# Performance work log

Hardware: AMD Instinct MI355X
Metric: run time of the kernel (lower is better)

## Reference

```python
import jax, jax.numpy as jnp
import numpy as np


def _lstm(x, Wih, Whh, b):
    # x: [B, T, D]; torch gate order (i, f, g, o); returns final (h, c)
    B = x.shape[0]
    H = Whh.shape[0]
    def step(carry, xt):
        h, c = carry
        gates = xt @ Wih + h @ Whh + b
        i, f, g, o = jnp.split(gates, 4, axis=-1)
        c = jax.nn.sigmoid(f) * c + jax.nn.sigmoid(i) * jnp.tanh(g)
        h = jax.nn.sigmoid(o) * jnp.tanh(c)
        return (h, c), None
    h0 = jnp.zeros((B, H), x.dtype)
    (h, c), _ = jax.lax.scan(step, (h0, h0), jnp.swapaxes(x, 0, 1))
    return h, c


def _bn(x, g, b, eps=1e-5):
    # BatchNorm1d training-mode math (biased variance over batch dim)
    m = x.mean(0)
    v = x.var(0)
    return (x - m) * jax.lax.rsqrt(v + eps) * g + b


def setup_inputs():
    L, N, C, D, H, HID = 16, 128, 10, 13, 128, 64
    F = 15 + 7 + 2 + HID  # 88, lstm2/composer input width
    key = jax.random.key(0)
    ks = jax.random.split(key, 20)
    def rn(i, shape, s=0.08):
        return jax.random.normal(ks[i], shape, jnp.float32) * s
    return {
        "operators": rn(0, (L, N, 15), 1.0),
        "extra_infos": rn(1, (L, N, 7), 1.0),
        "cardinalities": rn(2, (L, N, 2), 1.0),
        "condition1s": rn(3, (L, N, C, D), 1.0),
        "condition2s": rn(4, (L, N, C, D), 1.0),
        "mapping": jax.random.randint(ks[5], (L - 1, N, 2), 0, N + 1, jnp.int32),
        # lstm1
        "Wih1": rn(6, (D, 4 * H)), "Whh1": rn(7, (H, 4 * H)), "b1": jnp.zeros((4 * H,), jnp.float32),
        # condition_mlp + batch_norm1
        "Wc": rn(8, (H, HID)), "bc": jnp.zeros((HID,), jnp.float32),
        "g1": jnp.ones((HID,), jnp.float32), "be1": jnp.zeros((HID,), jnp.float32),
        # lstm2
        "Wih2": rn(9, (F, 4 * H)), "Whh2": rn(10, (H, 4 * H)), "b2": jnp.zeros((4 * H,), jnp.float32),
        # composer: input proj + 5 stacked (lh, rh) gate Linears, order [i, lf, rf, u, o]
        "Win": rn(11, (F, H)), "bin_": jnp.zeros((H,), jnp.float32),
        "Wlh": rn(12, (5, H, H)), "blh": jnp.zeros((5, H), jnp.float32),
        "Wrh": rn(13, (5, H, H)), "brh": jnp.zeros((5, H), jnp.float32),
        # head (task1 only; task2 branch is dead code in forward)
        "g2": jnp.ones((H,), jnp.float32), "be2": jnp.zeros((H,), jnp.float32),
        "Wt1": rn(14, (H, HID)), "bt1": jnp.zeros((HID,), jnp.float32),
        "g3": jnp.ones((HID,), jnp.float32), "be3": jnp.zeros((HID,), jnp.float32),
        "Wt2": rn(15, (HID, HID)), "bt2": jnp.zeros((HID,), jnp.float32),
        "Wo": rn(16, (HID, 1)), "bo": jnp.zeros((1,), jnp.float32),
    }


def _forward(operators, extra_infos, cardinalities, condition1s, condition2s, mapping,
             Wih1, Whh1, b1, Wc, bc, g1, be1, Wih2, Whh2, b2,
             Win, bin_, Wlh, blh, Wrh, brh,
             g2, be2, Wt1, bt1, g3, be3, Wt2, bt2, Wo, bo):
    L, N = operators.shape[0], operators.shape[1]
    H = Whh1.shape[0]
    # condition encoder: both condition tensors share lstm1 -> run batched together
    C, D = condition1s.shape[2], condition1s.shape[3]
    c_all = jnp.concatenate([condition1s, condition2s], 0).reshape(2 * L * N, C, D)
    h_all, _ = _lstm(c_all, Wih1, Whh1, b1)
    h1, h2 = jnp.split(h_all, 2, 0)
    lo = (jax.nn.relu(h1 @ Wc + bc) + jax.nn.relu(h2 @ Wc + bc)) * 0.5
    lo = _bn(lo, g1, be1).reshape(L, N, -1)
    out = jnp.concatenate([operators, extra_infos, cardinalities, lo], 2)  # [L, N, F]

    # leaf level through lstm2 (seq len 1, zero init)
    h0, c0 = _lstm(out[L - 1][:, None, :], Wih2, Whh2, b2)  # [N, H]
    # torch code broadcasts [N,1,H] input against [*,N,H] hidden -> state is [N,N,H];
    # pre-broadcasting the initial [1,N,H] state to [N,N,H] is value-identical and lets us scan.
    hid = jnp.broadcast_to(h0[None], (N, N, H))
    cid = jnp.broadcast_to(c0[None], (N, N, H))

    def step(carry, x):
        hid, cid = carry
        lvl, mp = x  # lvl: [N, F], mp: [N, 2] with values in [0, N] (0 = zero pad)
        pad = jnp.zeros((N, 1, H), hid.dtype)
        nh = jnp.concatenate([pad, hid], 1)  # [N, N+1, H]
        nc = jnp.concatenate([pad, cid], 1)
        lh, lc = nh[:, mp[:, 0]], nc[:, mp[:, 0]]  # [N, N, H]
        rh, rc = nh[:, mp[:, 1]], nc[:, mp[:, 1]]
        base = (lvl @ Win + bin_)[:, None, :]  # [N, 1, H] (computed once, reused for all 5 gates)
        pre = (base[None]
               + jnp.einsum('anh,ghk->gank', lh, Wlh) + blh[:, None, None, :]
               + jnp.einsum('anh,ghk->gank', rh, Wrh) + brh[:, None, None, :])  # [5, N, N, H]
        i = jax.nn.sigmoid(pre[0])
        lf = jax.nn.sigmoid(pre[1])
        rf = jax.nn.sigmoid(pre[2])
        u = jnp.tanh(pre[3])
        o = jax.nn.sigmoid(pre[4])
        c = i * u + lf * lc + rf * rc
        h = o * jnp.tanh(c)
        return (h, c), None

    (hid, cid), _ = jax.lax.scan(step, (hid, cid), (out[:L - 1][::-1], mapping[::-1]))
    output = hid[0]  # [N, H]; original slices [0:batch_size]=N here (randn operators are nonzero)
    t = _bn(output, g2, be2)
    t = jax.nn.relu(t @ Wt1 + bt1)
    t = _bn(t, g3, be3)
    t = jax.nn.relu(t @ Wt2 + bt2)
    return jax.nn.sigmoid(t @ Wo + bo)  # [N, 1]


def reference(operators, extra_infos, cardinalities, condition1s, condition2s, mapping,
              Wih1, Whh1, b1, Wc, bc, g1, be1, Wih2, Whh2, b2,
              Win, bin_, Wlh, blh, Wrh, brh,
              g2, be2, Wt1, bt1, g3, be3, Wt2, bt2, Wo, bo):
    return _forward(operators, extra_infos, cardinalities, condition1s, condition2s, mapping,
                    Wih1, Whh1, b1, Wc, bc, g1, be1, Wih2, Whh2, b2,
                    Win, bin_, Wlh, blh, Wrh, brh,
                    g2, be2, Wt1, bt1, g3, be3, Wt2, bt2, Wo, bo)
```

## Files before the change

kernel.cpp:

```cpp
#include <hip/hip_runtime.h>
#include <hip/hip_bf16.h>

__device__ __forceinline__ float sigf(float x) {
  return __fdividef(1.0f, 1.0f + __expf(-x));
}
__device__ __forceinline__ float tanhfast(float x) {
  float e = __expf(2.0f * x);
  return 1.0f - __fdividef(2.0f, e + 1.0f);
}

__global__ __launch_bounds__(256) void k_pre(
    const float* __restrict__ Whh1, const float* __restrict__ Wih1,
    const float* __restrict__ b1, const float* __restrict__ Wlh,
    const float* __restrict__ Wrh,
    float* __restrict__ WhhP, float* __restrict__ WihP,
    float* __restrict__ b1P, float* __restrict__ WT)
{
  const int bx = blockIdx.x, tid = threadIdx.x;
  if (bx < 32) {
    for (int i = 0; i < 8; ++i) {
      int dst = bx * 2048 + i * 256 + tid;
      int g = dst & 3, u = (dst >> 2) & 127, k = dst >> 9;
      WhhP[dst] = Whh1[k * 512 + g * 128 + u];
    }
  } else if (bx == 32) {
    for (int idx = tid; idx < 13 * 512; idx += 256) {
      int g = idx & 3, u = (idx >> 2) & 127, d = idx >> 9;
      WihP[idx] = Wih1[d * 512 + g * 128 + u];
    }
    for (int idx = tid; idx < 512; idx += 256)
      b1P[idx] = b1[(idx & 3) * 128 + (idx >> 2)];
  } else {
    __shared__ float tile[32][33];
    const int m = bx - 33;
    const int side = m / 5, g = m - side * 5;
    const float* src = (side ? Wrh : Wlh) + g * 16384;
    float* dst = WT + m * 16384;
    const int i = tid >> 5, jj = tid & 31;
    for (int tt = 0; tt < 16; ++tt) {
      const int ti = tt >> 2, tj = tt & 3;
#pragma unroll
      for (int q = 0; q < 4; ++q)
        tile[i + q * 8][jj] = src[(ti * 32 + i + q * 8) * 128 + tj * 32 + jj];
      __syncthreads();
#pragma unroll
      for (int q = 0; q < 4; ++q)
        dst[(tj * 32 + i + q * 8) * 128 + ti * 32 + jj] = tile[jj][i + q * 8];
      __syncthreads();
    }
  }
}

__global__ __launch_bounds__(512, 1) void k_lstm1(
    const float* __restrict__ cond1, const float* __restrict__ cond2,
    const float* __restrict__ WihP, const float* __restrict__ WhhP,
    const float* __restrict__ b1P, const float* __restrict__ Wc,
    const float* __restrict__ bc,
    float* __restrict__ lo_raw, float* __restrict__ gpartial)
{
  __shared__ float4 pS[4][8][128];
  __shared__ float4 hs4[16][32];
  __shared__ float  xs[16][132];
  __shared__ float4 WihS[13][128];
  __shared__ float  rr[16][64];
  __shared__ float  sloc[128];

  const int tid = threadIdx.x, b = blockIdx.x;
  const int u = tid & 127, rg = tid >> 7;

  for (int idx = tid; idx < 16 * 130; idx += 512) {
    int r = idx / 130, d = idx - r * 130;
    xs[r][d] = (r < 8) ? cond1[(8 * b + r) * 130 + d]
                       : cond2[(8 * b + (r - 8)) * 130 + d];
  }
  for (int idx = tid; idx < 13 * 128; idx += 512)
    WihS[idx >> 7][idx & 127] =
        *(const float4*)&WihP[(idx >> 7) * 512 + 4 * (idx & 127)];
  ((float4*)hs4)[tid] = make_float4(0.f, 0.f, 0.f, 0.f);
  if (tid < 128) sloc[tid] = 0.f;

  float4 w[32];
#pragma unroll
  for (int kk = 0; kk < 32; ++kk)
    w[kk] = *(const float4*)&WhhP[(32 * rg + kk) * 512 + 4 * u];
  const float4 b1v = *(const float4*)&b1P[4 * u];
  float creg[4] = {0.f, 0.f, 0.f, 0.f};
  __syncthreads();

  for (int t = 0; t < 10; ++t) {
#pragma unroll
    for (int hf = 0; hf < 2; ++hf) {
      const int base = 8 * hf;
#pragma unroll
      for (int row = 0; row < 8; ++row) {
        float4 a = make_float4(0.f, 0.f, 0.f, 0.f);
#pragma unroll
        for (int q = 0; q < 8; ++q) {
          const float4 hv = hs4[base + row][8 * rg + q];
          const float4 w0 = w[4 * q + 0], w1 = w[4 * q + 1];
          const float4 w2 = w[4 * q + 2], w3 = w[4 * q + 3];
          a.x = fmaf(hv.x, w0.x, a.x); a.y = fmaf(hv.x, w0.y, a.y);
          a.z = fmaf(hv.x, w0.z, a.z); a.w = fmaf(hv.x, w0.w, a.w);
          a.x = fmaf(hv.y, w1.x, a.x); a.y = fmaf(hv.y, w1.y, a.y);
          a.z = fmaf(hv.y, w1.z, a.z); a.w = fmaf(hv.y, w1.w, a.w);
          a.x = fmaf(hv.z, w2.x, a.x); a.y = fmaf(hv.z, w2.y, a.y);
          a.z = fmaf(hv.z, w2.z, a.z); a.w = fmaf(hv.z, w2.w, a.w);
          a.x = fmaf(hv.w, w3.x, a.x); a.y = fmaf(hv.w, w3.y, a.y);
          a.z = fmaf(hv.w, w3.z, a.z); a.w = fmaf(hv.w, w3.w, a.w);
        }
        pS[rg][row][u] = a;
      }
      __syncthreads();
      {
        float4 gs[2];
#pragma unroll
        for (int i = 0; i < 2; ++i) {
          const int rh = 2 * rg + i;
          float4 s0 = pS[0][rh][u], s1 = pS[1][rh][u];
          float4 s2 = pS[2][rh][u], s3 = pS[3][rh][u];
          gs[i].x = ((s0.x + s1.x) + (s2.x + s3.x)) + b1v.x;
          gs[i].y = ((s0.y + s1.y) + (s2.y + s3.y)) + b1v.y;
          gs[i].z = ((s0.z + s1.z) + (s2.z + s3.z)) + b1v.z;
          gs[i].w = ((s0.w + s1.w) + (s2.w + s3.w)) + b1v.w;
        }
#pragma unroll
        for (int d = 0; d < 13; ++d) {
          const float4 wv = WihS[d][u];
#pragma unroll
          for (int i = 0; i < 2; ++i) {
            const float xv = xs[base + 2 * rg + i][t * 13 + d];
            gs[i].x = fmaf(xv, wv.x, gs[i].x);
            gs[i].y = fmaf(xv, wv.y, gs[i].y);
            gs[i].z = fmaf(xv, wv.z, gs[i].z);
            gs[i].w = fmaf(xv, wv.w, gs[i].w);
          }
        }
#pragma unroll
        for (int i = 0; i < 2; ++i) {
          const int row = base + 2 * rg + i;
          const int ci = 2 * hf + i;
          float ig = sigf(gs[i].x);
          float fg = sigf(gs[i].y);
          float gg = tanhfast(gs[i].z);
          float og = sigf(gs[i].w);
          float c = fmaf(fg, creg[ci], ig * gg);
          creg[ci] = c;
          ((float*)&hs4[row][0])[u] = og * tanhfast(c);
        }
      }
      __syncthreads();
    }
  }

  {
    const int oc = tid & 63, r8 = tid >> 6;
    const float* h0 = (const float*)&hs4[2 * r8][0];
    const float* h1 = (const float*)&hs4[2 * r8 + 1][0];
    float a0 = bc[oc], a1 = a0;
    for (int k = 0; k < 128; ++k) {
      float wcv = Wc[k * 64 + oc];
      a0 = fmaf(h0[k], wcv, a0);
      a1 = fmaf(h1[k], wcv, a1);
    }
    rr[2 * r8][oc] = fmaxf(a0, 0.f);
    rr[2 * r8 + 1][oc] = fmaxf(a1, 0.f);
  }
  __syncthreads();
  {
    const int j = tid >> 6, oc = tid & 63;
    float lo = 0.5f * (rr[j][oc] + rr[j + 8][oc]);
    lo_raw[(8 * b + j) * 64 + oc] = lo;
    atomicAdd(&sloc[oc], lo);
    atomicAdd(&sloc[64 + oc], lo * lo);
  }
  __syncthreads();
  if (tid < 128) gpartial[tid * 256 + b] = sloc[tid];
}

__device__ __forceinline__ void bn1_scales(
    const float* __restrict__ gpartial, const float* __restrict__ g1,
    const float* __restrict__ be1, float* sS, float* av, float* bv)
{
  const int tid = threadIdx.x;
  if (tid < 128) {
    const float4* gp = (const float4*)(gpartial + tid * 256);
    float s = 0.f;
    for (int i = 0; i < 64; ++i) {
      float4 v = gp[i];
      s += (v.x + v.y) + (v.z + v.w);
    }
    sS[tid] = s;
  }
  __syncthreads();
  if (tid < 64) {
    float m = sS[tid] * (1.0f / 2048.0f);
    float var = sS[64 + tid] * (1.0f / 2048.0f) - m * m;
    float rstd = rsqrtf(var + 1e-5f);
    float gg = g1[tid];
    av[tid] = rstd * gg;
    bv[tid] = be1[tid] - m * rstd * gg;
  }
  __syncthreads();
}

__device__ __forceinline__ float feat(
    int l, int n, int f, const float* __restrict__ ops,
    const float* __restrict__ extra, const float* __restrict__ card,
    const float* __restrict__ lo_raw, const float* av, const float* bv)
{
  int g = l * 128 + n;
  if (f < 15) return ops[g * 15 + f];
  if (f < 22) return extra[g * 7 + (f - 15)];
  if (f < 24) return card[g * 2 + (f - 22)];
  int j = f - 24;
  return lo_raw[g * 64 + j] * av[j] + bv[j];
}

__global__ __launch_bounds__(256) void k_mid(
    const float* __restrict__ ops, const float* __restrict__ extra,
    const float* __restrict__ card, const float* __restrict__ lo_raw,
    const float* __restrict__ gpartial, const float* __restrict__ g1,
    const float* __restrict__ be1, const float* __restrict__ Wih2,
    const float* __restrict__ b2, const float* __restrict__ Win,
    const float* __restrict__ binb, float* __restrict__ hidA,
    float* __restrict__ cidA, float* __restrict__ base_all)
{
  __shared__ float sS[128], av[64], bv[64];
  __shared__ float X[2][88];
  const int tid = threadIdx.x, bx = blockIdx.x;
  bn1_scales(gpartial, g1, be1, sS, av, bv);

  if (bx < 64) {
    if (tid < 176) {
      int r = tid / 88, f = tid - r * 88;
      X[r][f] = feat(15, 2 * bx + r, f, ops, extra, card, lo_raw, av, bv);
    }
    __syncthreads();
    const int nl = tid >> 7, k = tid & 127;
    const float* Xr = X[nl];
    float ai = b2[k];
    float ag = b2[256 + k];
    float ao = b2[384 + k];
#pragma unroll 8
    for (int f = 0; f < 88; ++f) {
      float xv = Xr[f];
      ai = fmaf(xv, Wih2[f * 512 + k], ai);
      ag = fmaf(xv, Wih2[f * 512 + 256 + k], ag);
      ao = fmaf(xv, Wih2[f * 512 + 384 + k], ao);
    }
    float c0 = sigf(ai) * tanhfast(ag);
    float h0 = sigf(ao) * tanhfast(c0);
    const int idx = (2 * bx + nl) * 128 + k;
    hidA[idx] = h0;
    cidA[idx] = c0;
  } else {
    const int t = bx - 64;
    if (tid < 88)
      X[0][tid] = feat(t, 0, tid, ops, extra, card, lo_raw, av, bv);
    __syncthreads();
    if (tid < 128) {
      float a = binb[tid];
#pragma unroll 8
      for (int f = 0; f < 88; ++f)
        a = fmaf(X[0][f], Win[f * 128 + tid], a);
      base_all[t * 128 + tid] = a;
    }
  }
}

__global__ __launch_bounds__(512, 1) void k_tree(
    const int* __restrict__ mapping, const float* __restrict__ WT,
    const float* __restrict__ base_all, const float* __restrict__ blh,
    const float* __restrict__ brh, const float* __restrict__ hid_c,
    const float* __restrict__ cid_c, float* __restrict__ hid_n,
    float* __restrict__ cid_n, int t)
{
  __shared__ float wS[10][8][132];
  __shared__ float rowS[64][132];
  __shared__ float pS[10][264];
  const int tid = threadIdx.x, bx = blockIdx.x;
  const int k0 = (bx & 15) * 8, n0 = (bx >> 4) * 32;

  for (int idx = tid; idx < 10 * 8 * 128; idx += 512) {
    int h = idx & 127, kp = (idx >> 7) & 7, sg = idx >> 10;
    wS[sg][kp][h] = WT[sg * 16384 + (k0 + kp) * 128 + h];
  }
  for (int idx = tid; idx < 64 * 128; idx += 512) {
    int row = idx >> 7, h = idx & 127;
    int np_ = row >> 1, side = row & 1;
    int j = mapping[(t * 128 + n0 + np_) * 2 + side];
    rowS[row][h] = (j > 0) ? hid_c[(j - 1) * 128 + h] : 0.0f;
  }
  __syncthreads();

  {
    const int pr = tid >> 1, side = tid & 1;
    const int np_ = pr >> 3, kp = pr & 7;
    const int rrow = np_ * 2 + side;
    float acc[5] = {0.f, 0.f, 0.f, 0.f, 0.f};
    for (int h = 0; h < 128; h += 8) {
      float4 r0 = *(const float4*)&rowS[rrow][h];
      float4 r1 = *(const float4*)&rowS[rrow][h + 4];
#pragma unroll
      for (int g = 0; g < 5; ++g) {
        float4 w0 = *(const float4*)&wS[side * 5 + g][kp][h];
        float4 w1 = *(const float4*)&wS[side * 5 + g][kp][h + 4];
        acc[g] = fmaf(r0.x, w0.x, acc[g]);
        acc[g] = fmaf(r0.y, w0.y, acc[g]);
        acc[g] = fmaf(r0.z, w0.z, acc[g]);
        acc[g] = fmaf(r0.w, w0.w, acc[g]);
        acc[g] = fmaf(r1.x, w1.x, acc[g]);
        acc[g] = fmaf(r1.y, w1.y, acc[g]);
        acc[g] = fmaf(r1.z, w1.z, acc[g]);
        acc[g] = fmaf(r1.w, w1.w, acc[g]);
      }
    }
#pragma unroll
    for (int g = 0; g < 5; ++g) pS[side * 5 + g][pr] = acc[g];
  }
  __syncthreads();
  if (tid < 256) {
    const int np_ = tid >> 3, kp = tid & 7;
    const int n = n0 + np_, k = k0 + kp;
    const float base = base_all[t * 128 + k];
    float pre[5];
#pragma unroll
    for (int g = 0; g < 5; ++g)
      pre[g] = pS[g][tid] + pS[5 + g][tid] + base +
               blh[g * 128 + k] + brh[g * 128 + k];
    int jl = mapping[(t * 128 + n) * 2 + 0];
    int jr = mapping[(t * 128 + n) * 2 + 1];
    float lc = (jl > 0) ? cid_c[(jl - 1) * 128 + k] : 0.0f;
    float rc = (jr > 0) ? cid_c[(jr - 1) * 128 + k] : 0.0f;
    float i_ = sigf(pre[0]);
    float lf = sigf(pre[1]);
    float rf = sigf(pre[2]);
    float u_ = tanhfast(pre[3]);
    float o_ = sigf(pre[4]);
    float c = i_ * u_ + lf * lc + rf * rc;
    hid_n[n * 128 + k] = o_ * tanhfast(c);
    cid_n[n * 128 + k] = c;
  }
}

__global__ __launch_bounds__(512) void k_head(
    const float* __restrict__ hid, const float* __restrict__ g2,
    const float* __restrict__ be2, const float* __restrict__ Wt1,
    const float* __restrict__ bt1, const float* __restrict__ g3,
    const float* __restrict__ be3, const float* __restrict__ Wt2,
    const float* __restrict__ bt2, const float* __restrict__ Wo,
    const float* __restrict__ bo, float* __restrict__ dout)
{
  __shared__ __align__(16) unsigned char pool[32768 + 16384];
  __hip_bfloat16 (*t1s)[128] = (__hip_bfloat16(*)[128])pool;
  __hip_bfloat16 (*t2s)[64]  = (__hip_bfloat16(*)[64])(pool + 32768);
  float (*t4s)[64] = (float(*)[64])pool;
  __shared__ float red[8][128];
  __shared__ float av[128], bv[128];
  const int tid = threadIdx.x;

  {
    int k = tid & 127, q = tid >> 7;
    float s = 0.f, s2 = 0.f;
    for (int r = q * 32; r < q * 32 + 32; ++r) {
      float v = hid[r * 128 + k];
      s += v; s2 += v * v;
    }
    red[q][k] = s;
    red[4 + q][k] = s2;
  }
  __syncthreads();
  if (tid < 128) {
    float s = red[0][tid] + red[1][tid] + red[2][tid] + red[3][tid];
    float s2 = red[4][tid] + red[5][tid] + red[6][tid] + red[7][tid];
    float m = s * (1.0f / 128.0f);
    float var = s2 * (1.0f / 128.0f) - m * m;
    float rstd = rsqrtf(var + 1e-5f);
    float gg = g2[tid];
    av[tid] = rstd * gg;
    bv[tid] = be2[tid] - m * rstd * gg;
  }
  __syncthreads();
  for (int idx = tid; idx < 16384; idx += 512) {
    int n = idx >> 7, k = idx & 127;
    t1s[n][k] = __float2bfloat16(hid[idx] * av[k] + bv[k]);
  }
  __syncthreads();
  {
    const int j = tid & 63, ng = tid >> 6;
    float a[16];
#pragma unroll
    for (int r = 0; r < 16; ++r) a[r] = bt1[j];
    for (int k8 = 0; k8 < 128; k8 += 8) {
      float wv[8];
#pragma unroll
      for (int q = 0; q < 8; ++q) wv[q] = Wt1[(k8 + q) * 64 + j];
#pragma unroll
      for (int r = 0; r < 16; ++r) {
        const __hip_bfloat16* row = &t1s[ng * 16 + r][k8];
#pragma unroll
        for (int q = 0; q < 8; ++q)
          a[r] = fmaf(__bfloat162float(row[q]), wv[q], a[r]);
      }
    }
#pragma unroll
    for (int r = 0; r < 16; ++r)
      t2s[ng * 16 + r][j] = __float2bfloat16(fmaxf(a[r], 0.0f));
  }
  __syncthreads();
  {
    int j = tid & 63, q = tid >> 6;
    float s = 0.f, s2 = 0.f;
    for (int r = q * 16; r < q * 16 + 16; ++r) {
      float v = __bfloat162float(t2s[r][j]);
      s += v; s2 += v * v;
    }
    red[q][j] = s;
    red[q][64 + j] = s2;
  }
  __syncthreads();
  if (tid < 64) {
    float s = 0.f, s2 = 0.f;
#pragma unroll
    for (int q = 0; q < 8; ++q) { s += red[q][tid]; s2 += red[q][64 + tid]; }
    float m = s * (1.0f / 128.0f);
    float var = s2 * (1.0f / 128.0f) - m * m;
    float rstd = rsqrtf(var + 1e-5f);
    float gg = g3[tid];
    av[tid] = rstd * gg;
    bv[tid] = be3[tid] - m * rstd * gg;
  }
  __syncthreads();
  {
    const int j2 = tid & 63, ng = tid >> 6;
    float a[16];
#pragma unroll
    for (int r = 0; r < 16; ++r) a[r] = bt2[j2];
    for (int jj = 0; jj < 64; ++jj) {
      float w = Wt2[jj * 64 + j2];
      float aj = av[jj], bj = bv[jj];
#pragma unroll
      for (int r = 0; r < 16; ++r) {
        float x = __bfloat162float(t2s[ng * 16 + r][jj]) * aj + bj;
        a[r] = fmaf(x, w, a[r]);
      }
    }
    __syncthreads();
#pragma unroll
    for (int r = 0; r < 16; ++r) t4s[ng * 16 + r][j2] = fmaxf(a[r], 0.0f);
  }
  __syncthreads();
  if (tid < 128) {
    float a = bo[0];
    for (int j = 0; j < 64; ++j) a = fmaf(t4s[tid][j], Wo[j], a);
    dout[tid] = sigf(a);
  }
}

extern "C" void kernel_launch(void* const* d_in, const int* in_sizes, int n_in,
                              void* d_out, int out_size, void* d_ws,
                              size_t ws_size, hipStream_t stream)
{
  (void)in_sizes; (void)n_in; (void)out_size; (void)ws_size;
  const float* ops   = (const float*)d_in[0];
  const float* extra = (const float*)d_in[1];
  const float* card  = (const float*)d_in[2];
  const float* cond1 = (const float*)d_in[3];
  const float* cond2 = (const float*)d_in[4];
  const int* mapping = (const int*)d_in[5];
  const float* Wih1 = (const float*)d_in[6];
  const float* Whh1 = (const float*)d_in[7];
  const float* b1   = (const float*)d_in[8];
  const float* Wc   = (const float*)d_in[9];
  const float* bc   = (const float*)d_in[10];
  const float* g1   = (const float*)d_in[11];
  const float* be1  = (const float*)d_in[12];
  const float* Wih2 = (const float*)d_in[13];
  const float* b2   = (const float*)d_in[15];
  const float* Win  = (const float*)d_in[16];
  const float* binb = (const float*)d_in[17];
  const float* Wlh  = (const float*)d_in[18];
  const float* blh  = (const float*)d_in[19];
  const float* Wrh  = (const float*)d_in[20];
  const float* brh  = (const float*)d_in[21];
  const float* g2   = (const float*)d_in[22];
  const float* be2  = (const float*)d_in[23];
  const float* Wt1  = (const float*)d_in[24];
  const float* bt1  = (const float*)d_in[25];
  const float* g3   = (const float*)d_in[26];
  const float* be3  = (const float*)d_in[27];
  const float* Wt2  = (const float*)d_in[28];
  const float* bt2  = (const float*)d_in[29];
  const float* Wo   = (const float*)d_in[30];
  const float* bo   = (const float*)d_in[31];

  char* ws = (char*)d_ws;
  float* WhhP     = (float*)(ws + 0);
  float* WihP     = (float*)(ws + 262144);
  float* b1P      = (float*)(ws + 288768);
  float* gpartial = (float*)(ws + 290816);
  float* lo_raw   = (float*)(ws + 421888);
  float* base_all = (float*)(ws + 946176);
  float* WT       = (float*)(ws + 953856);
  float* hidA     = (float*)(ws + 1609216);
  float* hidB     = hidA + 16384;
  float* cidA     = hidB + 16384;
  float* cidB     = cidA + 16384;

  k_pre<<<dim3(43), dim3(256), 0, stream>>>(
      Whh1, Wih1, b1, Wlh, Wrh, WhhP, WihP, b1P, WT);
  k_lstm1<<<dim3(256), dim3(512), 0, stream>>>(
      cond1, cond2, WihP, WhhP, b1P, Wc, bc, lo_raw, gpartial);
  k_mid<<<dim3(79), dim3(256), 0, stream>>>(
      ops, extra, card, lo_raw, gpartial, g1, be1, Wih2, b2, Win, binb,
      hidA, cidA, base_all);

  float* hc[2] = {hidA, hidB};
  float* cc[2] = {cidA, cidB};
  for (int s = 0; s < 15; ++s) {
    int t = 14 - s;
    int cur = s & 1, nxt = cur ^ 1;
    k_tree<<<dim3(64), dim3(512), 0, stream>>>(
        mapping, WT, base_all, blh, brh,
        hc[cur], cc[cur], hc[nxt], cc[nxt], t);
  }
  k_head<<<dim3(1), dim3(512), 0, stream>>>(
      hc[1], g2, be2, Wt1, bt1, g3, be3, Wt2, bt2, Wo, bo,
      (float*)d_out);
}
```

Before: 445.3 us.

## Move LSTM1 recurrence onto bf16 split-precision MFMA and simplify tree kernel reduction

```diff
diff --git a/kernel.cpp b/kernel.cpp
--- a/kernel.cpp
+++ b/kernel.cpp
@@ -1,5 +1,9 @@
 #include <hip/hip_runtime.h>
 #include <hip/hip_bf16.h>
+
+typedef __attribute__((ext_vector_type(8))) short short8v;
+typedef __attribute__((ext_vector_type(4))) short short4v;
+typedef __attribute__((ext_vector_type(4))) float f32x4;
 
 __device__ __forceinline__ float sigf(float x) {
   return __fdividef(1.0f, 1.0f + __expf(-x));
@@ -8,31 +12,39 @@
   float e = __expf(2.0f * x);
   return 1.0f - __fdividef(2.0f, e + 1.0f);
 }
+__device__ __forceinline__ unsigned short rne_bf16(float x) {
+  unsigned u = __float_as_uint(x);
+  return (unsigned short)((u + 0x7fffu + ((u >> 16) & 1u)) >> 16);
+}
+__device__ __forceinline__ float bf2f(unsigned short s) {
+  return __uint_as_float(((unsigned)s) << 16);
+}
 
 __global__ __launch_bounds__(256) void k_pre(
     const float* __restrict__ Whh1, const float* __restrict__ Wih1,
-    const float* __restrict__ b1, const float* __restrict__ Wlh,
-    const float* __restrict__ Wrh,
-    float* __restrict__ WhhP, float* __restrict__ WihP,
-    float* __restrict__ b1P, float* __restrict__ WT)
+    const float* __restrict__ Wlh, const float* __restrict__ Wrh,
+    unsigned short* __restrict__ Bft, float* __restrict__ WT)
 {
   const int bx = blockIdx.x, tid = threadIdx.x;
-  if (bx < 32) {
-    for (int i = 0; i < 8; ++i) {
-      int dst = bx * 2048 + i * 256 + tid;
-      int g = dst & 3, u = (dst >> 2) & 127, k = dst >> 9;
-      WhhP[dst] = Whh1[k * 512 + g * 128 + u];
-    }
-  } else if (bx == 32) {
-    for (int idx = tid; idx < 13 * 512; idx += 256) {
-      int g = idx & 3, u = (idx >> 2) & 127, d = idx >> 9;
-      WihP[idx] = Wih1[d * 512 + g * 128 + u];
-    }
-    for (int idx = tid; idx < 512; idx += 256)
-      b1P[idx] = b1[(idx & 3) * 128 + (idx >> 2)];
+  if (bx < 40) {
+    for (int i = 0; i < 16; ++i) {
+      int idx = (bx * 256 + tid) * 16 + i;
+      int p = (idx >= 81920) ? 1 : 0;
+      int r = idx - p * 81920;
+      int q = r >> 14;
+      int rem = r & 16383;
+      int ct = rem >> 9, l = (rem >> 3) & 63, e = rem & 7;
+      int kk = 32 * q + ((l >> 4) << 3) + e;
+      int col = (ct << 4) + (l & 15);
+      float x = 0.f;
+      if (kk < 128) x = Whh1[kk * 512 + col];
+      else if (kk < 141) x = Wih1[(kk - 128) * 512 + col];
+      unsigned short hi = rne_bf16(x);
+      Bft[idx] = p ? rne_bf16(x - bf2f(hi)) : hi;
+    }
   } else {
     __shared__ float tile[32][33];
-    const int m = bx - 33;
+    const int m = bx - 40;
     const int side = m / 5, g = m - side * 5;
     const float* src = (side ? Wrh : Wlh) + g * 16384;
     float* dst = WT + m * 16384;
@@ -53,114 +65,146 @@
 
 __global__ __launch_bounds__(512, 1) void k_lstm1(
     const float* __restrict__ cond1, const float* __restrict__ cond2,
-    const float* __restrict__ WihP, const float* __restrict__ WhhP,
-    const float* __restrict__ b1P, const float* __restrict__ Wc,
-    const float* __restrict__ bc,
+    const unsigned short* __restrict__ Bft, const float* __restrict__ b1,
+    const float* __restrict__ Wc, const float* __restrict__ bc,
     float* __restrict__ lo_raw, float* __restrict__ gpartial)
 {
-  __shared__ float4 pS[4][8][128];
-  __shared__ float4 hs4[16][32];
-  __shared__ float  xs[16][132];
-  __shared__ float4 WihS[13][128];
-  __shared__ float  rr[16][64];
-  __shared__ float  sloc[128];
+  __shared__ __align__(16) unsigned short AftS[2][5][64][8];
+  __shared__ float preS[16][516];
+  __shared__ float xs[16][132];
+  __shared__ float hsF[16][132];
+  __shared__ float rr[16][64];
+  __shared__ float sloc[128];
 
   const int tid = threadIdx.x, b = blockIdx.x;
-  const int u = tid & 127, rg = tid >> 7;
+  const int wid = tid >> 6, lane = tid & 63;
 
   for (int idx = tid; idx < 16 * 130; idx += 512) {
     int r = idx / 130, d = idx - r * 130;
     xs[r][d] = (r < 8) ? cond1[(8 * b + r) * 130 + d]
                        : cond2[(8 * b + (r - 8)) * 130 + d];
   }
-  for (int idx = tid; idx < 13 * 128; idx += 512)
-    WihS[idx >> 7][idx & 127] =
-        *(const float4*)&WihP[(idx >> 7) * 512 + 4 * (idx & 127)];
-  ((float4*)hs4)[tid] = make_float4(0.f, 0.f, 0.f, 0.f);
+  for (int idx = tid; idx < 2560; idx += 512) ((unsigned*)AftS)[idx] = 0u;
   if (tid < 128) sloc[tid] = 0.f;
 
-  float4 w[32];
-#pragma unroll
-  for (int kk = 0; kk < 32; ++kk)
-    w[kk] = *(const float4*)&WhhP[(32 * rg + kk) * 512 + 4 * u];
-  const float4 b1v = *(const float4*)&b1P[4 * u];
+  short8v Bh[5][4], Bl[5][4];
+  {
+    const short8v* gB = (const short8v*)Bft;
+#pragma unroll
+    for (int q = 0; q < 5; ++q)
+#pragma unroll
+      for (int j = 0; j < 4; ++j) {
+        int ct = 4 * wid + j;
+        Bh[q][j] = gB[(q * 32 + ct) * 64 + lane];
+        Bl[q][j] = gB[((5 + q) * 32 + ct) * 64 + lane];
+      }
+  }
+  float biasv[4];
+#pragma unroll
+  for (int j = 0; j < 4; ++j) biasv[j] = b1[(4 * wid + j) * 16 + (lane & 15)];
+
+  const int grow = tid >> 5;
+  const int guu = (tid & 31) * 4;
   float creg[4] = {0.f, 0.f, 0.f, 0.f};
+
+  __syncthreads();
+  if (tid < 256) {
+    int p = tid >> 7, s = tid & 127, row = s & 15, grp = s >> 4;
+    {
+      float v = xs[row][grp];
+      unsigned short hi = rne_bf16(v);
+      AftS[p][4][row][grp] = p ? rne_bf16(v - bf2f(hi)) : hi;
+    }
+    if (grp < 5) {
+      float v = xs[row][8 + grp];
+      unsigned short hi = rne_bf16(v);
+      AftS[p][4][16 + row][grp] = p ? rne_bf16(v - bf2f(hi)) : hi;
+    }
+  }
   __syncthreads();
 
   for (int t = 0; t < 10; ++t) {
-#pragma unroll
-    for (int hf = 0; hf < 2; ++hf) {
-      const int base = 8 * hf;
-#pragma unroll
-      for (int row = 0; row < 8; ++row) {
-        float4 a = make_float4(0.f, 0.f, 0.f, 0.f);
-#pragma unroll
-        for (int q = 0; q < 8; ++q) {
-          const float4 hv = hs4[base + row][8 * rg + q];
-          const float4 w0 = w[4 * q + 0], w1 = w[4 * q + 1];
-          const float4 w2 = w[4 * q + 2], w3 = w[4 * q + 3];
-          a.x = fmaf(hv.x, w0.x, a.x); a.y = fmaf(hv.x, w0.y, a.y);
-          a.z = fmaf(hv.x, w0.z, a.z); a.w = fmaf(hv.x, w0.w, a.w);
-          a.x = fmaf(hv.y, w1.x, a.x); a.y = fmaf(hv.y, w1.y, a.y);
-          a.z = fmaf(hv.y, w1.z, a.z); a.w = fmaf(hv.y, w1.w, a.w);
-          a.x = fmaf(hv.z, w2.x, a.x); a.y = fmaf(hv.z, w2.y, a.y);
-          a.z = fmaf(hv.z, w2.z, a.z); a.w = fmaf(hv.z, w2.w, a.w);
-          a.x = fmaf(hv.w, w3.x, a.x); a.y = fmaf(hv.w, w3.y, a.y);
-          a.z = fmaf(hv.w, w3.z, a.z); a.w = fmaf(hv.w, w3.w, a.w);
-        }
-        pS[rg][row][u] = a;
-      }
-      __syncthreads();
+    f32x4 acc[4];
+#pragma unroll
+    for (int j = 0; j < 4; ++j)
+      acc[j] = (f32x4){biasv[j], biasv[j], biasv[j], biasv[j]};
+#pragma unroll
+    for (int q = 0; q < 5; ++q) {
+      short8v ah = *(const short8v*)&AftS[0][q][lane][0];
+      short8v al = *(const short8v*)&AftS[1][q][lane][0];
+#pragma unroll
+      for (int j = 0; j < 4; ++j) {
+        acc[j] = __builtin_amdgcn_mfma_f32_16x16x32_bf16(al, Bh[q][j],
+                                                         acc[j], 0, 0, 0);
+        acc[j] = __builtin_amdgcn_mfma_f32_16x16x32_bf16(ah, Bl[q][j],
+                                                         acc[j], 0, 0, 0);
+        acc[j] = __builtin_amdgcn_mfma_f32_16x16x32_bf16(ah, Bh[q][j],
+                                                         acc[j], 0, 0, 0);
+      }
+    }
+#pragma unroll
+    for (int j = 0; j < 4; ++j) {
+      int c = (4 * wid + j) * 16 + (lane & 15);
+      int r0 = (lane >> 4) * 4;
+#pragma unroll
+      for (int r = 0; r < 4; ++r) preS[r0 + r][c] = acc[j][r];
+    }
+    __syncthreads();
+    {
+      float4 pi = *(const float4*)&preS[grow][0 * 128 + guu];
+      float4 pf = *(const float4*)&preS[grow][1 * 128 + guu];
+      float4 pg = *(const float4*)&preS[grow][2 * 128 + guu];
+      float4 po = *(const float4*)&preS[grow][3 * 128 + guu];
+      float hv[4];
+#pragma unroll
+      for (int i2 = 0; i2 < 4; ++i2) {
+        float ig = sigf(((const float*)&pi)[i2]);
+        float fg = sigf(((const float*)&pf)[i2]);
+        float gg = tanhfast(((const float*)&pg)[i2]);
+        float og = sigf(((const float*)&po)[i2]);
+        float c = fmaf(fg, creg[i2], ig * gg);
+        creg[i2] = c;
+        hv[i2] = og * tanhfast(c);
+      }
+      *(float4*)&hsF[grow][guu] = make_float4(hv[0], hv[1], hv[2], hv[3]);
+      unsigned short h0 = rne_bf16(hv[0]), h1 = rne_bf16(hv[1]);
+      unsigned short h2 = rne_bf16(hv[2]), h3 = rne_bf16(hv[3]);
+      short4v hiv = (short4v){(short)h0, (short)h1, (short)h2, (short)h3};
+      short4v lov = (short4v){(short)rne_bf16(hv[0] - bf2f(h0)),
+                              (short)rne_bf16(hv[1] - bf2f(h1)),
+                              (short)rne_bf16(hv[2] - bf2f(h2)),
+                              (short)rne_bf16(hv[3] - bf2f(h3))};
+      int chunk = guu >> 5;
+      int lA = grow + 16 * ((guu >> 3) & 3);
+      int e0 = guu & 7;
+      *(short4v*)&AftS[0][chunk][lA][e0] = hiv;
+      *(short4v*)&AftS[1][chunk][lA][e0] = lov;
+    }
+    if (t < 9 && tid < 256) {
+      int p = tid >> 7, s = tid & 127, row = s & 15, grp = s >> 4;
       {
-        float4 gs[2];
-#pragma unroll
-        for (int i = 0; i < 2; ++i) {
-          const int rh = 2 * rg + i;
-          float4 s0 = pS[0][rh][u], s1 = pS[1][rh][u];
-          float4 s2 = pS[2][rh][u], s3 = pS[3][rh][u];
-          gs[i].x = ((s0.x + s1.x) + (s2.x + s3.x)) + b1v.x;
-          gs[i].y = ((s0.y + s1.y) + (s2.y + s3.y)) + b1v.y;
-          gs[i].z = ((s0.z + s1.z) + (s2.z + s3.z)) + b1v.z;
-          gs[i].w = ((s0.w + s1.w) + (s2.w + s3.w)) + b1v.w;
-        }
-#pragma unroll
-        for (int d = 0; d < 13; ++d) {
-          const float4 wv = WihS[d][u];
-#pragma unroll
-          for (int i = 0; i < 2; ++i) {
-            const float xv = xs[base + 2 * rg + i][t * 13 + d];
-            gs[i].x = fmaf(xv, wv.x, gs[i].x);
-            gs[i].y = fmaf(xv, wv.y, gs[i].y);
-            gs[i].z = fmaf(xv, wv.z, gs[i].z);
-            gs[i].w = fmaf(xv, wv.w, gs[i].w);
-          }
-        }
-#pragma unroll
-        for (int i = 0; i < 2; ++i) {
-          const int row = base + 2 * rg + i;
-          const int ci = 2 * hf + i;
-          float ig = sigf(gs[i].x);
-          float fg = sigf(gs[i].y);
-          float gg = tanhfast(gs[i].z);
-          float og = sigf(gs[i].w);
-          float c = fmaf(fg, creg[ci], ig * gg);
-          creg[ci] = c;
-          ((float*)&hs4[row][0])[u] = og * tanhfast(c);
-        }
-      }
-      __syncthreads();
-    }
+        float v = xs[row][(t + 1) * 13 + grp];
+        unsigned short hi = rne_bf16(v);
+        AftS[p][4][row][grp] = p ? rne_bf16(v - bf2f(hi)) : hi;
+      }
+      if (grp < 5) {
+        float v = xs[row][(t + 1) * 13 + 8 + grp];
+        unsigned short hi = rne_bf16(v);
+        AftS[p][4][16 + row][grp] = p ? rne_bf16(v - bf2f(hi)) : hi;
+      }
+    }
+    __syncthreads();
   }
 
   {
     const int oc = tid & 63, r8 = tid >> 6;
-    const float* h0 = (const float*)&hs4[2 * r8][0];
-    const float* h1 = (const float*)&hs4[2 * r8 + 1][0];
+    const float* h0p = &hsF[2 * r8][0];
+    const float* h1p = &hsF[2 * r8 + 1][0];
     float a0 = bc[oc], a1 = a0;
     for (int k = 0; k < 128; ++k) {
       float wcv = Wc[k * 64 + oc];
-      a0 = fmaf(h0[k], wcv, a0);
-      a1 = fmaf(h1[k], wcv, a1);
+      a0 = fmaf(h0p[k], wcv, a0);
+      a1 = fmaf(h1p[k], wcv, a1);
     }
     rr[2 * r8][oc] = fmaxf(a0, 0.f);
     rr[2 * r8 + 1][oc] = fmaxf(a1, 0.f);
@@ -277,15 +321,14 @@
 {
   __shared__ float wS[10][8][132];
   __shared__ float rowS[64][132];
-  __shared__ float pS[10][264];
   const int tid = threadIdx.x, bx = blockIdx.x;
   const int k0 = (bx & 15) * 8, n0 = (bx >> 4) * 32;
 
-  for (int idx = tid; idx < 10 * 8 * 128; idx += 512) {
+  for (int idx = tid; idx < 10240; idx += 512) {
     int h = idx & 127, kp = (idx >> 7) & 7, sg = idx >> 10;
     wS[sg][kp][h] = WT[sg * 16384 + (k0 + kp) * 128 + h];
   }
-  for (int idx = tid; idx < 64 * 128; idx += 512) {
+  for (int idx = tid; idx < 8192; idx += 512) {
     int row = idx >> 7, h = idx & 127;
     int np_ = row >> 1, side = row & 1;
     int j = mapping[(t * 128 + n0 + np_) * 2 + side];
@@ -293,51 +336,48 @@
   }
   __syncthreads();
 
-  {
-    const int pr = tid >> 1, side = tid & 1;
-    const int np_ = pr >> 3, kp = pr & 7;
-    const int rrow = np_ * 2 + side;
-    float acc[5] = {0.f, 0.f, 0.f, 0.f, 0.f};
-    for (int h = 0; h < 128; h += 8) {
-      float4 r0 = *(const float4*)&rowS[rrow][h];
-      float4 r1 = *(const float4*)&rowS[rrow][h + 4];
-#pragma unroll
-      for (int g = 0; g < 5; ++g) {
-        float4 w0 = *(const float4*)&wS[side * 5 + g][kp][h];
-        float4 w1 = *(const float4*)&wS[side * 5 + g][kp][h + 4];
-        acc[g] = fmaf(r0.x, w0.x, acc[g]);
-        acc[g] = fmaf(r0.y, w0.y, acc[g]);
-        acc[g] = fmaf(r0.z, w0.z, acc[g]);
-        acc[g] = fmaf(r0.w, w0.w, acc[g]);
-        acc[g] = fmaf(r1.x, w1.x, acc[g]);
-        acc[g] = fmaf(r1.y, w1.y, acc[g]);
-        acc[g] = fmaf(r1.z, w1.z, acc[g]);
-        acc[g] = fmaf(r1.w, w1.w, acc[g]);
-      }
-    }
-#pragma unroll
-    for (int g = 0; g < 5; ++g) pS[side * 5 + g][pr] = acc[g];
-  }
-  __syncthreads();
-  if (tid < 256) {
-    const int np_ = tid >> 3, kp = tid & 7;
-    const int n = n0 + np_, k = k0 + kp;
-    const float base = base_all[t * 128 + k];
-    float pre[5];
-#pragma unroll
-    for (int g = 0; g < 5; ++g)
-      pre[g] = pS[g][tid] + pS[5 + g][tid] + base +
-               blh[g * 128 + k] + brh[g * 128 + k];
-    int jl = mapping[(t * 128 + n) * 2 + 0];
-    int jr = mapping[(t * 128 + n) * 2 + 1];
-    float lc = (jl > 0) ? cid_c[(jl - 1) * 128 + k] : 0.0f;
-    float rc = (jr > 0) ? cid_c[(jr - 1) * 128 + k] : 0.0f;
-    float i_ = sigf(pre[0]);
-    float lf = sigf(pre[1]);
-    float rf = sigf(pre[2]);
-    float u_ = tanhfast(pre[3]);
-    float o_ = sigf(pre[4]);
-    float c = i_ * u_ + lf * lc + rf * rc;
+  const int wid = tid >> 6, lane = tid & 63;
+  const int kp = wid, k = k0 + kp;
+  const int np_ = lane >> 1, side = lane & 1, n = n0 + np_;
+
+  float acc[5] = {0.f, 0.f, 0.f, 0.f, 0.f};
+  const float* rp = &rowS[lane][0];
+  for (int h = 0; h < 128; h += 8) {
+    float4 r0 = *(const float4*)&rp[h];
+    float4 r1 = *(const float4*)&rp[h + 4];
+#pragma unroll
+    for (int g = 0; g < 5; ++g) {
+      float4 w0 = *(const float4*)&wS[side * 5 + g][kp][h];
+      float4 w1 = *(const float4*)&wS[side * 5 + g][kp][h + 4];
+      acc[g] = fmaf(r0.x, w0.x, acc[g]);
+      acc[g] = fmaf(r0.y, w0.y, acc[g]);
+      acc[g] = fmaf(r0.z, w0.z, acc[g]);
+      acc[g] = fmaf(r0.w, w0.w, acc[g]);
+      acc[g] = fmaf(r1.x, w1.x, acc[g]);
+      acc[g] = fmaf(r1.y, w1.y, acc[g]);
+      acc[g] = fmaf(r1.z, w1.z, acc[g]);
+      acc[g] = fmaf(r1.w, w1.w, acc[g]);
+    }
+  }
+#pragma unroll
+  for (int g = 0; g < 5; ++g) acc[g] += __shfl_xor(acc[g], 1);
+
+  const float base = base_all[t * 128 + k];
+  float pre[5];
+#pragma unroll
+  for (int g = 0; g < 5; ++g)
+    pre[g] = acc[g] + base + blh[g * 128 + k] + brh[g * 128 + k];
+  int jl = mapping[(t * 128 + n) * 2 + 0];
+  int jr = mapping[(t * 128 + n) * 2 + 1];
+  float lc = (jl > 0) ? cid_c[(jl - 1) * 128 + k] : 0.0f;
+  float rc = (jr > 0) ? cid_c[(jr - 1) * 128 + k] : 0.0f;
+  float i_ = sigf(pre[0]);
+  float lf = sigf(pre[1]);
+  float rf = sigf(pre[2]);
+  float u_ = tanhfast(pre[3]);
+  float o_ = sigf(pre[4]);
+  float c = i_ * u_ + lf * lc + rf * rc;
+  if (side == 0) {
     hid_n[n * 128 + k] = o_ * tanhfast(c);
     cid_n[n * 128 + k] = c;
   }
@@ -495,22 +535,19 @@
   const float* bo   = (const float*)d_in[31];
 
   char* ws = (char*)d_ws;
-  float* WhhP     = (float*)(ws + 0);
-  float* WihP     = (float*)(ws + 262144);
-  float* b1P      = (float*)(ws + 288768);
-  float* gpartial = (float*)(ws + 290816);
-  float* lo_raw   = (float*)(ws + 421888);
-  float* base_all = (float*)(ws + 946176);
-  float* WT       = (float*)(ws + 953856);
-  float* hidA     = (float*)(ws + 1609216);
+  unsigned short* Bft = (unsigned short*)(ws + 0);
+  float* gpartial = (float*)(ws + 327680);
+  float* lo_raw   = (float*)(ws + 458752);
+  float* base_all = (float*)(ws + 983040);
+  float* WT       = (float*)(ws + 990720);
+  float* hidA     = (float*)(ws + 1646080);
   float* hidB     = hidA + 16384;
   float* cidA     = hidB + 16384;
   float* cidB     = cidA + 16384;
 
-  k_pre<<<dim3(43), dim3(256), 0, stream>>>(
-      Whh1, Wih1, b1, Wlh, Wrh, WhhP, WihP, b1P, WT);
+  k_pre<<<dim3(50), dim3(256), 0, stream>>>(Whh1, Wih1, Wlh, Wrh, Bft, WT);
   k_lstm1<<<dim3(256), dim3(512), 0, stream>>>(
-      cond1, cond2, WihP, WhhP, b1P, Wc, bc, lo_raw, gpartial);
+      cond1, cond2, Bft, b1, Wc, bc, lo_raw, gpartial);
   k_mid<<<dim3(79), dim3(256), 0, stream>>>(
       ops, extra, card, lo_raw, gpartial, g1, be1, Wih2, b2, Win, binb,
       hidA, cidA, base_all);
```

Result: faster. 394.0 us (-11.5%).
